# Kernel tuning notes

Hardware: AMD Instinct MI355X
Metric: run time of the kernel (lower is better)

Reference implementation:

```python
import jax, jax.numpy as jnp
import numpy as np
import math

NEG = -1e32
B, S, D, H, DFF, L = 16, 512, 1024, 8, 4096, 3
DK = D // H


def layernorm(x, g, b, eps=1e-5):
    mu = x.mean(-1, keepdims=True)
    var = ((x - mu) ** 2).mean(-1, keepdims=True)
    return (x - mu) / jnp.sqrt(var + eps) * g + b


def gen_dam(alphas, E, bmask):
    # alphas, E: [H, S, 2]; hard gumbel-softmax with straight-through
    Hh, Ss, _ = alphas.shape
    g = -jnp.log(E + 1e-5)
    y_soft = jax.nn.softmax(alphas + g, axis=-1)  # tau = 1
    idx = jnp.argmax(y_soft, axis=-1)
    y_hard = jax.nn.one_hot(idx, 2, dtype=y_soft.dtype)
    m = y_hard - jax.lax.stop_gradient(y_soft) + y_soft
    m = jnp.broadcast_to(m[:, :, 0:1], (Hh, Ss, Ss))
    m = jnp.triu(m)
    m = jnp.rot90(m, 1, axes=(1, 2))
    i = jnp.arange(Ss)[:, None]
    j = jnp.arange(Ss)[None, :]
    src = jnp.clip(j - i, 0, Ss - 1)
    shifted = m[:, jnp.arange(Ss)[:, None], src]  # mask_tri[:, i, j] = m[:, i, j - i]
    mask_tri = jnp.where(j >= i, shifted, 0.0)
    masks = mask_tri + jnp.swapaxes(jnp.triu(mask_tri, 1), 1, 2)
    masks = jnp.triu(masks, bmask)
    return masks


def attention(q, k, v, src_mask, dam, zero_pad, gammas):
    # q,k,v: [B,H,S,dk]; src_mask: [S,S] bool; dam: [H,S,S] bool
    dk = q.shape[-1]
    Ss = q.shape[2]
    scores = jnp.einsum('bhqd,bhkd->bhqk', q, k) / math.sqrt(dk)
    damb = dam[None]          # [1,H,S,S]
    smb = src_mask[None, None]  # [1,1,S,S]
    # NOTE: faithful to the torch code, where the first masked_fill(mask==0)
    # result is overwritten - only dam masks the first softmax.
    sc = jnp.where(damb, scores, NEG)
    sc = jax.nn.softmax(sc, axis=-1)
    sc = sc * smb.astype(sc.dtype) * damb.astype(sc.dtype)
    distcum = jnp.cumsum(sc, axis=-1)
    disttot = jnp.sum(sc, axis=-1, keepdims=True)
    pos = jnp.abs(jnp.arange(Ss)[None, :] - jnp.arange(Ss)[:, None]).astype(scores.dtype)
    dist = jnp.sqrt(jnp.clip((disttot - distcum) * pos[None, None], 0.0, None))
    dist = jax.lax.stop_gradient(dist)
    gamma = -jax.nn.softplus(gammas)[None]  # [1,H,1,1]
    te = jnp.clip(jnp.exp(dist * gamma), 1e-5, 1e5)
    scores = scores * te
    scores = jnp.where(smb, scores, NEG)
    scores = jnp.where(damb, scores, NEG)
    scores = jax.nn.softmax(scores, axis=-1)
    if zero_pad:
        scores = scores.at[:, :, 0, :].set(0.0)
    return jnp.einsum('bhqk,bhkd->bhqd', scores, v)


def transformer_layer(bmask, query, key, values, apply_pos, p):
    Bb, Ss, Dd = query.shape
    Hh = p['gammas'].shape[0]
    dam = gen_dam(p['alphas'], p['E'], bmask) == 0
    src_mask = jnp.triu(jnp.ones((Ss, Ss), jnp.int32), bmask) == 0
    k = (key @ p['kW'].T + p['kb']).reshape(Bb, Ss, Hh, -1).transpose(0, 2, 1, 3)
    q = (query @ p['kW'].T + p['kb']).reshape(Bb, Ss, Hh, -1).transpose(0, 2, 1, 3)  # kq_same
    v = (values @ p['vW'].T + p['vb']).reshape(Bb, Ss, Hh, -1).transpose(0, 2, 1, 3)
    att = attention(q, k, v, src_mask, dam, bmask == 0, p['gammas'])
    concat = att.transpose(0, 2, 1, 3).reshape(Bb, Ss, Dd)
    q2 = concat @ p['oW'].T + p['ob']
    x = layernorm(query + q2, p['ln1_g'], p['ln1_b'])
    if apply_pos:
        ff = jax.nn.relu(x @ p['w1'].T + p['b1']) @ p['w2'].T + p['b2']
        x = layernorm(x + ff, p['ln2_g'], p['ln2_b'])
    return x


def setup_inputs() -> dict:
    key = jax.random.key(0)
    ks = jax.random.split(key, 16)
    sc = 0.02
    return {
        'q_embed_data': jax.random.normal(ks[0], (B, S, D), jnp.float32),
        'qa_embed_data': jax.random.normal(ks[1], (B, S, D), jnp.float32),
        'kW': sc * jax.random.normal(ks[2], (L, D, D), jnp.float32),
        'kb': jnp.zeros((L, D), jnp.float32),
        'vW': sc * jax.random.normal(ks[3], (L, D, D), jnp.float32),
        'vb': jnp.zeros((L, D), jnp.float32),
        'oW': sc * jax.random.normal(ks[4], (L, D, D), jnp.float32),
        'ob': jnp.zeros((L, D), jnp.float32),
        'gammas': 0.5 * jax.random.normal(ks[5], (L, H, 1, 1), jnp.float32),
        'alphas': 0.001 * jax.random.normal(ks[6], (L, H, S, 2), jnp.float32),
        'ln1_g': jnp.ones((L, D), jnp.float32),
        'ln1_b': jnp.zeros((L, D), jnp.float32),
        'w1': sc * jax.random.normal(ks[7], (L, DFF, D), jnp.float32),
        'b1': jnp.zeros((L, DFF), jnp.float32),
        'w2': sc * jax.random.normal(ks[8], (L, D, DFF), jnp.float32),
        'b2': jnp.zeros((L, D), jnp.float32),
        'ln2_g': jnp.ones((L, D), jnp.float32),
        'ln2_b': jnp.zeros((L, D), jnp.float32),
        'gumbel_E': jax.random.exponential(ks[9], (L, H, S, 2), jnp.float32),
    }


def reference(q_embed_data, qa_embed_data, kW, kb, vW, vb, oW, ob, gammas,
              alphas, ln1_g, ln1_b, w1, b1, w2, b2, ln2_g, ln2_b, gumbel_E):
    def P(l):
        return {'kW': kW[l], 'kb': kb[l], 'vW': vW[l], 'vb': vb[l],
                'oW': oW[l], 'ob': ob[l], 'gammas': gammas[l], 'alphas': alphas[l],
                'ln1_g': ln1_g[l], 'ln1_b': ln1_b[l], 'w1': w1[l], 'b1': b1[l],
                'w2': w2[l], 'b2': b2[l], 'ln2_g': ln2_g[l], 'ln2_b': ln2_b[l],
                'E': gumbel_E[l]}
    # blocks_1: self-attention over answer embedding (mask=1)
    y = transformer_layer(1, qa_embed_data, qa_embed_data, qa_embed_data, True, P(0))
    # blocks_2: self-attn on question emb (no FFN), then cross-attn into y
    x = transformer_layer(1, q_embed_data, q_embed_data, q_embed_data, False, P(1))
    x = transformer_layer(0, x, x, y, True, P(2))
    return x
```

## Files before the change

kernel.cpp:

```cpp
#include <hip/hip_runtime.h>
#include <math.h>

#define NEGV -1e32f

typedef __bf16 bf16_t;
typedef _Float16 f16_t;
typedef __bf16 bf16x8 __attribute__((ext_vector_type(8)));
typedef __bf16 bf16x4 __attribute__((ext_vector_type(4)));
typedef _Float16 f16x8 __attribute__((ext_vector_type(8)));
typedef float floatx4 __attribute__((ext_vector_type(4)));

static __device__ __forceinline__ float fexp(float x) { return __expf(x); }
#if __has_builtin(__builtin_amdgcn_sqrtf)
static __device__ __forceinline__ float fsqrt(float x) { return __builtin_amdgcn_sqrtf(x); }
#else
static __device__ __forceinline__ float fsqrt(float x) { return sqrtf(x); }
#endif
#if __has_builtin(__builtin_amdgcn_rcpf)
static __device__ __forceinline__ float frcp(float x) { return __builtin_amdgcn_rcpf(x); }
#else
static __device__ __forceinline__ float frcp(float x) { return 1.0f / x; }
#endif

static __device__ __forceinline__ float wave_sum(float v) {
#pragma unroll
  for (int d = 32; d > 0; d >>= 1) v += __shfl_xor(v, d, 64);
  return v;
}
static __device__ __forceinline__ float wave_max(float v) {
#pragma unroll
  for (int d = 32; d > 0; d >>= 1) v = fmaxf(v, __shfl_xor(v, d, 64));
  return v;
}

static __device__ __forceinline__ void gl2lds16(const bf16_t* g, bf16_t* l) {
  __builtin_amdgcn_global_load_lds((__attribute__((address_space(1))) void*)(void*)g,
                                   (__attribute__((address_space(3))) void*)l, 16, 0, 0);
}

template <int WM, int WN, int FM, int FN, int BIAS_MODE, bool RELU, int OUT_MODE>
__global__ __launch_bounds__(WM * WN * 64) void gemm_db(
    const bf16_t* __restrict__ A, long lda, long a_so, long a_si,
    const bf16_t* __restrict__ B, long ldb, long b_so, long b_si,
    void* __restrict__ Cv, long ldc, long c_so, long c_si,
    const float* __restrict__ bias, int zdiv, int K, float alpha)
{
  constexpr int THREADS = WM * WN * 64;
  constexpr int BM = WM * FM * 16;
  constexpr int BN = WN * FN * 16;
  constexpr int RR = THREADS / 8;
  constexpr int RA = BM / RR;
  constexpr int RB = BN / RR;
  constexpr int NSTG = RA + RB;
  extern __shared__ bf16_t smem[];
  bf16_t* const Asb = smem;
  bf16_t* const Bsb = smem + 2 * (BM * 64);

  const int tid = threadIdx.x;
  const int wave = tid >> 6;
  const int lane = tid & 63;
  const int wm = wave / WN;
  const int wn = wave % WN;
  const int z = blockIdx.z;
  const long zo = z / zdiv;
  const long zi = z % zdiv;
  A += zo * a_so + zi * a_si;
  B += zo * b_so + zi * b_si;
  const long m0 = (long)blockIdx.x * BM;
  const long n0 = (long)blockIdx.y * BN;

  const int srow = tid >> 3;
  const int scol = ((tid & 7) ^ (srow & 7)) * 8;
  const bf16_t* gA = A + (m0 + srow) * lda + scol;
  const bf16_t* gB = B + (n0 + srow) * ldb + scol;
  const int lofs = wave * 512;

  floatx4 acc[FM][FN] = {};
  const int lr = lane & 15;
  const int kg = lane >> 4;
  const int NT = K >> 6;

  {
    bf16_t* lA = Asb + lofs;
    bf16_t* lB = Bsb + lofs;
#pragma unroll
    for (int r = 0; r < RA; ++r) gl2lds16(gA + (long)(r * RR) * lda, lA + r * RR * 64);
#pragma unroll
    for (int r = 0; r < RB; ++r) gl2lds16(gB + (long)(r * RR) * ldb, lB + r * RR * 64);
  }

  for (int t = 0; t < NT; ++t) {
    const int buf = t & 1;
    if (t + 1 < NT) {
      const long ko = (long)(t + 1) * 64;
      bf16_t* lA = Asb + (buf ^ 1) * (BM * 64) + lofs;
      bf16_t* lB = Bsb + (buf ^ 1) * (BN * 64) + lofs;
#pragma unroll
      for (int r = 0; r < RA; ++r) gl2lds16(gA + (long)(r * RR) * lda + ko, lA + r * RR * 64);
#pragma unroll
      for (int r = 0; r < RB; ++r) gl2lds16(gB + (long)(r * RR) * ldb + ko, lB + r * RR * 64);
      asm volatile("s_waitcnt vmcnt(%0)" :: "n"(NSTG) : "memory");
    } else {
      asm volatile("s_waitcnt vmcnt(0)" ::: "memory");
    }
    __builtin_amdgcn_s_barrier();
    __builtin_amdgcn_sched_barrier(0);
    const bf16_t* __restrict__ Ab = Asb + buf * (BM * 64);
    const bf16_t* __restrict__ Bb = Bsb + buf * (BN * 64);
#pragma unroll
    for (int h = 0; h < 2; ++h) {
      const int slot = ((h * 4 + kg) ^ (lr & 7)) * 8;
      bf16x8 af[FM], bfr[FN];
#pragma unroll
      for (int m = 0; m < FM; ++m)
        af[m] = *(const bf16x8*)(Ab + (wm * (FM * 16) + m * 16 + lr) * 64 + slot);
#pragma unroll
      for (int n = 0; n < FN; ++n)
        bfr[n] = *(const bf16x8*)(Bb + (wn * (FN * 16) + n * 16 + lr) * 64 + slot);
#pragma unroll
      for (int m = 0; m < FM; ++m)
#pragma unroll
        for (int n = 0; n < FN; ++n)
          acc[m][n] = __builtin_amdgcn_mfma_f32_16x16x32_bf16(af[m], bfr[n], acc[m][n], 0, 0, 0);
    }
    __builtin_amdgcn_sched_barrier(0);
    __builtin_amdgcn_s_barrier();
  }

  const long coff = zo * c_so + zi * c_si;
  const int q4 = (lane >> 4) * 4;
#pragma unroll
  for (int m = 0; m < FM; ++m) {
#pragma unroll
    for (int n = 0; n < FN; ++n) {
#pragma unroll
      for (int r = 0; r < 4; ++r) {
        const long row = m0 + wm * (FM * 16) + m * 16 + q4 + r;
        const long col = n0 + wn * (FN * 16) + n * 16 + lr;
        float v = acc[m][n][r] * alpha;
        if (BIAS_MODE == 1) v += bias[col];
        if (BIAS_MODE == 2) v += bias[row];
        if (RELU) v = fmaxf(v, 0.0f);
        const long idx = coff + row * ldc + col;
        if (OUT_MODE == 1)      ((bf16_t*)Cv)[idx] = (bf16_t)v;
        else if (OUT_MODE == 2) ((f16_t*)Cv)[idx]  = (f16_t)v;
        else                    ((float*)Cv)[idx]  = v;
      }
    }
  }
}

template <int BIAS_MODE, bool RELU, int OUT_MODE>
__global__ __launch_bounds__(256) void gemm_bt(
    const bf16_t* __restrict__ A, long lda, long a_so, long a_si,
    const bf16_t* __restrict__ B, long ldb, long b_so, long b_si,
    void* __restrict__ Cv, long ldc, long c_so, long c_si,
    const float* __restrict__ bias, int zdiv, int K, float alpha)
{
  __shared__ bf16_t As[8192];
  __shared__ bf16_t Bs[8192];
  const int tid = threadIdx.x;
  const int wave = tid >> 6;
  const int lane = tid & 63;
  const int wr = wave >> 1;
  const int wc = wave & 1;
  const int z = blockIdx.z;
  const long zo = z / zdiv;
  const long zi = z % zdiv;
  A += zo * a_so + zi * a_si;
  B += zo * b_so + zi * b_si;
  const long m0 = (long)blockIdx.x * 128;
  const long n0 = (long)blockIdx.y * 128;

  const int srow = tid >> 3;
  const int scol = ((tid & 7) ^ (srow & 7)) * 8;
  const bf16_t* gA = A + (m0 + srow) * lda + scol;
  const bf16_t* gB = B + (n0 + srow) * ldb + scol;
  bf16_t* lA = As + wave * 512;
  bf16_t* lB = Bs + wave * 512;

  floatx4 acc[4][4] = {};
  const int lr = lane & 15;
  const int kg = lane >> 4;

  for (int k0 = 0; k0 < K; k0 += 64) {
#pragma unroll
    for (int r = 0; r < 4; ++r) {
      gl2lds16(gA + (long)r * 32 * lda + k0, lA + r * 2048);
      gl2lds16(gB + (long)r * 32 * ldb + k0, lB + r * 2048);
    }
    __syncthreads();
#pragma unroll
    for (int h = 0; h < 2; ++h) {
      const int slot = ((h * 4 + kg) ^ (lr & 7)) * 8;
      bf16x8 af[4], bfr[4];
#pragma unroll
      for (int t = 0; t < 4; ++t) {
        af[t]  = *(const bf16x8*)(As + (wr * 64 + t * 16 + lr) * 64 + slot);
        bfr[t] = *(const bf16x8*)(Bs + (wc * 64 + t * 16 + lr) * 64 + slot);
      }
#pragma unroll
      for (int tm = 0; tm < 4; ++tm)
#pragma unroll
        for (int tn = 0; tn < 4; ++tn)
          acc[tm][tn] = __builtin_amdgcn_mfma_f32_16x16x32_bf16(af[tm], bfr[tn], acc[tm][tn], 0, 0, 0);
    }
    __syncthreads();
  }

  const long coff = zo * c_so + zi * c_si;
  const int q4 = (lane >> 4) * 4;
#pragma unroll
  for (int tm = 0; tm < 4; ++tm) {
#pragma unroll
    for (int tn = 0; tn < 4; ++tn) {
#pragma unroll
      for (int r = 0; r < 4; ++r) {
        const long row = m0 + wr * 64 + tm * 16 + q4 + r;
        const long col = n0 + wc * 64 + tn * 16 + lr;
        float v = acc[tm][tn][r] * alpha;
        if (BIAS_MODE == 1) v += bias[col];
        if (BIAS_MODE == 2) v += bias[row];
        if (RELU) v = fmaxf(v, 0.0f);
        const long idx = coff + row * ldc + col;
        if (OUT_MODE == 1)      ((bf16_t*)Cv)[idx] = (bf16_t)v;
        else if (OUT_MODE == 2) ((f16_t*)Cv)[idx]  = (f16_t)v;
        else                    ((float*)Cv)[idx]  = v;
      }
    }
  }
}

__global__ __launch_bounds__(256) void cast_kernel(const float* __restrict__ in,
                                                   bf16_t* __restrict__ out, long n)
{
  const long i = ((long)blockIdx.x * 256 + threadIdx.x) * 4;
  if (i >= n) return;
  const float4 v = *(const float4*)(in + i);
  bf16x4 o;
  o[0] = (bf16_t)v.x; o[1] = (bf16_t)v.y; o[2] = (bf16_t)v.z; o[3] = (bf16_t)v.w;
  *(bf16x4*)(out + i) = o;
}

__global__ void bbit_kernel(const float* __restrict__ alphas, const float* __restrict__ E,
                            int* __restrict__ bbit, int n)
{
  const int i = blockIdx.x * 256 + threadIdx.x;
  if (i >= n) return;
  const float l0 = alphas[2 * i]     - logf(E[2 * i]     + 1e-5f);
  const float l1 = alphas[2 * i + 1] - logf(E[2 * i + 1] + 1e-5f);
  bbit[i] = (l0 >= l1) ? 1 : 0;
}

template <bool XBF>
__global__ __launch_bounds__(256) void ln_kernel(
    const void* __restrict__ Xv, const float* __restrict__ R,
    const float* __restrict__ g, const float* __restrict__ b,
    float* __restrict__ out32, bf16_t* __restrict__ out16)
{
  const long row = blockIdx.x;
  const int t = threadIdx.x;
  float x0, x1, x2, x3;
  if (XBF) {
    const bf16x4 xv = *(const bf16x4*)((const bf16_t*)Xv + row * 1024 + t * 4);
    x0 = (float)xv[0]; x1 = (float)xv[1]; x2 = (float)xv[2]; x3 = (float)xv[3];
  } else {
    const float4 xv = *(const float4*)((const float*)Xv + row * 1024 + t * 4);
    x0 = xv.x; x1 = xv.y; x2 = xv.z; x3 = xv.w;
  }
  const float4 rv = *(const float4*)(R + row * 1024 + t * 4);
  const float v0 = x0 + rv.x, v1 = x1 + rv.y, v2 = x2 + rv.z, v3 = x3 + rv.w;
  float s  = v0 + v1 + v2 + v3;
  float s2 = v0 * v0 + v1 * v1 + v2 * v2 + v3 * v3;
  s = wave_sum(s); s2 = wave_sum(s2);
  __shared__ float red[8];
  const int wv = t >> 6, lane = t & 63;
  if (lane == 0) { red[wv] = s; red[4 + wv] = s2; }
  __syncthreads();
  s  = red[0] + red[1] + red[2] + red[3];
  s2 = red[4] + red[5] + red[6] + red[7];
  const float mu = s * (1.0f / 1024.0f);
  const float var = s2 * (1.0f / 1024.0f) - mu * mu;
  const float rstd = rsqrtf(var + 1e-5f);
  const float4 gv = *(const float4*)(g + t * 4);
  const float4 bv = *(const float4*)(b + t * 4);
  float4 ov;
  ov.x = (v0 - mu) * rstd * gv.x + bv.x;
  ov.y = (v1 - mu) * rstd * gv.y + bv.y;
  ov.z = (v2 - mu) * rstd * gv.z + bv.z;
  ov.w = (v3 - mu) * rstd * gv.w + bv.w;
  if (out32) *(float4*)(out32 + row * 1024 + t * 4) = ov;
  if (out16) {
    bf16x4 oh;
    oh[0] = (bf16_t)ov.x; oh[1] = (bf16_t)ov.y; oh[2] = (bf16_t)ov.z; oh[3] = (bf16_t)ov.w;
    *(bf16x4*)(out16 + row * 1024 + t * 4) = oh;
  }
}

__global__ __launch_bounds__(256) void attn_mid(
    const f16_t* __restrict__ S, bf16_t* __restrict__ P,
    const int* __restrict__ bbit, const float* __restrict__ gam,
    const int bmask, const int zero_pad)
{
  const int wid = threadIdx.x >> 6;
  const int lane = threadIdx.x & 63;
  const long rowid = (long)blockIdx.x * 4 + wid;
  const int i = (int)(rowid & 511);
  const int h = (int)(rowid >> 9) & 7;
  const f16_t* s = S + rowid * 512;
  const int jb = lane * 8;

  const float gv = gam[h];
  const float gamma = -log1pf(fexp(gv));

  float sv[8];
  {
    const f16x8 a = *(const f16x8*)(s + jb);
#pragma unroll
    for (int u = 0; u < 8; ++u) sv[u] = (float)a[u];
  }
  const int* bb = bbit + h * 512;
  float z[8];
  bool band[8];
  float m1 = NEGV;
#pragma unroll
  for (int u = 0; u < 8; ++u) {
    const int j = jb + u;
    const bool bd = j < i + bmask;
    band[u] = bd;
    int d = j - i; d = d < 0 ? 0 : d;
    const bool allowed = bd || (bb[d] == 0);
    z[u] = allowed ? sv[u] : NEGV;
    m1 = fmaxf(m1, z[u]);
  }
  m1 = wave_max(m1);
  float e[8], es = 0.f;
#pragma unroll
  for (int u = 0; u < 8; ++u) { e[u] = fexp(z[u] - m1); es += e[u]; }
  es = wave_sum(es);
  const float inv1 = frcp(es);

  float c[8];
  float run = 0.f;
#pragma unroll
  for (int u = 0; u < 8; ++u) {
    const float p = band[u] ? e[u] * inv1 : 0.f;
    run += p;
    c[u] = run;
  }
  float x = run;
#pragma unroll
  for (int d = 1; d < 64; d <<= 1) {
    const float y = __shfl_up(x, (unsigned)d, 64);
    if (lane >= d) x += y;
  }
  const float tot = __shfl(x, 63, 64);
  const float ex = x - run;

  float z2[8];
  float m2 = NEGV;
#pragma unroll
  for (int u = 0; u < 8; ++u) {
    const int j = jb + u;
    const float cc = c[u] + ex;
    const float pos = fabsf((float)(i - j));
    const float dist = fsqrt(fmaxf((tot - cc) * pos, 0.f));
    float te = fexp(dist * gamma);
    te = fminf(fmaxf(te, 1e-5f), 1e5f);
    z2[u] = band[u] ? sv[u] * te : NEGV;
    m2 = fmaxf(m2, z2[u]);
  }
  m2 = wave_max(m2);
  float f[8], es2 = 0.f;
#pragma unroll
  for (int u = 0; u < 8; ++u) { f[u] = fexp(z2[u] - m2); es2 += f[u]; }
  es2 = wave_sum(es2);
  const float inv2 = (zero_pad && i == 0) ? 0.f : frcp(es2);
  bf16x8 o;
#pragma unroll
  for (int u = 0; u < 8; ++u) o[u] = (bf16_t)(f[u] * inv2);
  *(bf16x8*)(P + rowid * 512 + jb) = o;
}

extern "C" void kernel_launch(void* const* d_in, const int* in_sizes, int n_in,
                              void* d_out, int out_size, void* d_ws, size_t ws_size,
                              hipStream_t stream)
{
  (void)in_sizes; (void)n_in; (void)out_size; (void)ws_size;
  const float* q_emb  = (const float*)d_in[0];
  const float* qa_emb = (const float*)d_in[1];
  const float* kW = (const float*)d_in[2];
  const float* kb = (const float*)d_in[3];
  const float* vW = (const float*)d_in[4];
  const float* vb = (const float*)d_in[5];
  const float* oW = (const float*)d_in[6];
  const float* ob = (const float*)d_in[7];
  const float* gammas = (const float*)d_in[8];
  const float* alphas = (const float*)d_in[9];
  const float* ln1_g = (const float*)d_in[10];
  const float* ln1_b = (const float*)d_in[11];
  const float* w1 = (const float*)d_in[12];
  const float* b1 = (const float*)d_in[13];
  const float* w2 = (const float*)d_in[14];
  const float* b2 = (const float*)d_in[15];
  const float* ln2_g = (const float*)d_in[16];
  const float* ln2_b = (const float*)d_in[17];
  const float* gumE = (const float*)d_in[18];
  float* outp = (float*)d_out;

  static bool attr_done = false;
  if (!attr_done) {
    attr_done = true;
    (void)hipFuncSetAttribute(reinterpret_cast<const void*>(&gemm_db<2,2,4,4,1,false,1>),
                              hipFuncAttributeMaxDynamicSharedMemorySize, 65536);
    (void)hipFuncSetAttribute(reinterpret_cast<const void*>(&gemm_db<2,2,4,4,2,false,1>),
                              hipFuncAttributeMaxDynamicSharedMemorySize, 65536);
    (void)hipFuncSetAttribute(reinterpret_cast<const void*>(&gemm_db<2,2,4,4,0,false,1>),
                              hipFuncAttributeMaxDynamicSharedMemorySize, 65536);
    (void)hipFuncSetAttribute(reinterpret_cast<const void*>(&gemm_db<2,2,4,4,1,false,0>),
                              hipFuncAttributeMaxDynamicSharedMemorySize, 65536);
    (void)hipFuncSetAttribute(reinterpret_cast<const void*>(&gemm_db<2,4,8,4,1,true,1>),
                              hipFuncAttributeMaxDynamicSharedMemorySize, 131072);
  }

  const size_t MBc = 1ull << 20;
  char* W = (char*)d_ws;
  int*    bbit = (int*)W;
  bf16_t* VB   = (bf16_t*)(W + 1 * MBc);
  bf16_t* XB   = (bf16_t*)(W + 17 * MBc);
  bf16_t* kWb  = (bf16_t*)(W + 33 * MBc);
  bf16_t* vWb  = (bf16_t*)(W + 39 * MBc);
  bf16_t* oWb  = (bf16_t*)(W + 45 * MBc);
  bf16_t* w1b  = (bf16_t*)(W + 51 * MBc);
  bf16_t* w2b  = (bf16_t*)(W + 59 * MBc);
  bf16_t* KQB  = (bf16_t*)(W + 67 * MBc);
  bf16_t* VT   = (bf16_t*)(W + 83 * MBc);
  f16_t*  SSPP = (f16_t*)(W + 99 * MBc);
  bf16_t* PPb  = (bf16_t*)(W + 99 * MBc);
  bf16_t* ATT  = (bf16_t*)(W + 163 * MBc);
  float*  O32  = (float*)(W + 67 * MBc);
  bf16_t* X1B  = (bf16_t*)(W + 99 * MBc);
  bf16_t* H1B  = (bf16_t*)(W + 115 * MBc);

  const long ND = 8388608;

  auto run_layer = [&](int l, const void* Qin, bool qin_bf16, const bf16_t* XBp,
                       const bf16_t* VBp, bool apply_pos, int bmask,
                       float* o32, bf16_t* o16) {
    const bf16_t* kWl = kWb + (long)l * 1048576;
    const bf16_t* vWl = vWb + (long)l * 1048576;
    const bf16_t* oWl = oWb + (long)l * 1048576;
    gemm_db<2,2,4,4,1,false,1><<<dim3(64, 8, 1), dim3(256), 65536, stream>>>(
        XBp, 1024, 0, 0, kWl, 1024, 0, 0, (void*)KQB, 1024, 0, 0,
        kb + l * 1024, 1, 1024, 1.0f);
    gemm_db<2,2,4,4,2,false,1><<<dim3(8, 4, 16), dim3(256), 65536, stream>>>(
        vWl, 1024, 0, 0, VBp, 1024, 524288, 0, (void*)VT, 512, 524288, 0,
        vb + l * 1024, 1, 1024, 1.0f);
    const int zp = (bmask == 0) ? 1 : 0;
    gemm_bt<0, false, 2><<<dim3(4, 4, 128), dim3(256), 0, stream>>>(
        KQB, 1024, 524288, 128, KQB, 1024, 524288, 128,
        (void*)SSPP, 512, 2097152, 262144, nullptr, 8, 128, 0.08838834764831845f);
    attn_mid<<<dim3(16384), dim3(256), 0, stream>>>(
        SSPP, PPb, bbit + l * 4096, gammas + l * 8, bmask, zp);
    gemm_db<2,2,4,4,0,false,1><<<dim3(4, 1, 128), dim3(256), 65536, stream>>>(
        PPb, 512, 2097152, 262144, VT, 512, 524288, 65536,
        (void*)ATT, 1024, 524288, 128, nullptr, 8, 512, 1.0f);
    gemm_db<2,2,4,4,1,false,0><<<dim3(64, 8, 1), dim3(256), 65536, stream>>>(
        ATT, 1024, 0, 0, oWl, 1024, 0, 0, (void*)O32, 1024, 0, 0,
        ob + l * 1024, 1, 1024, 1.0f);
    if (!apply_pos) {
      if (qin_bf16)
        ln_kernel<true><<<dim3(8192), dim3(256), 0, stream>>>(
            Qin, O32, ln1_g + l * 1024, ln1_b + l * 1024, o32, o16);
      else
        ln_kernel<false><<<dim3(8192), dim3(256), 0, stream>>>(
            Qin, O32, ln1_g + l * 1024, ln1_b + l * 1024, o32, o16);
    } else {
      cast_kernel<<<dim3(4096), dim3(256), 0, stream>>>(w1 + (long)l * 4194304, w1b, 4194304);
      cast_kernel<<<dim3(4096), dim3(256), 0, stream>>>(w2 + (long)l * 4194304, w2b, 4194304);
      if (qin_bf16)
        ln_kernel<true><<<dim3(8192), dim3(256), 0, stream>>>(
            Qin, O32, ln1_g + l * 1024, ln1_b + l * 1024, nullptr, X1B);
      else
        ln_kernel<false><<<dim3(8192), dim3(256), 0, stream>>>(
            Qin, O32, ln1_g + l * 1024, ln1_b + l * 1024, nullptr, X1B);
      gemm_db<2,4,8,4,1,true,1><<<dim3(32, 16, 1), dim3(512), 131072, stream>>>(
          X1B, 1024, 0, 0, w1b, 1024, 0, 0, (void*)H1B, 4096, 0, 0,
          b1 + l * 4096, 1, 1024, 1.0f);
      gemm_db<2,2,4,4,1,false,0><<<dim3(64, 8, 1), dim3(256), 65536, stream>>>(
          H1B, 4096, 0, 0, w2b, 4096, 0, 0, (void*)O32, 1024, 0, 0,
          b2 + l * 1024, 1, 4096, 1.0f);
      ln_kernel<true><<<dim3(8192), dim3(256), 0, stream>>>(
          X1B, O32, ln2_g + l * 1024, ln2_b + l * 1024, o32, o16);
    }
  };

  bbit_kernel<<<dim3(48), dim3(256), 0, stream>>>(alphas, gumE, bbit, 12288);
  cast_kernel<<<dim3(3072), dim3(256), 0, stream>>>(kW, kWb, 3145728);
  cast_kernel<<<dim3(3072), dim3(256), 0, stream>>>(vW, vWb, 3145728);
  cast_kernel<<<dim3(3072), dim3(256), 0, stream>>>(oW, oWb, 3145728);

  cast_kernel<<<dim3(8192), dim3(256), 0, stream>>>(qa_emb, XB, ND);
  run_layer(0, qa_emb, false, XB, XB, true, 1, nullptr, VB);
  cast_kernel<<<dim3(8192), dim3(256), 0, stream>>>(q_emb, XB, ND);
  run_layer(1, q_emb, false, XB, XB, false, 1, nullptr, XB);
  run_layer(2, XB, true, XB, VB, true, 0, outp, nullptr);
}
```

Measured before the change: 1.109 ms.

## Interleave global-to-LDS prefetch rounds with MFMA phases in GEMM main loop

```diff
diff --git a/kernel.cpp b/kernel.cpp
--- a/kernel.cpp
+++ b/kernel.cpp
@@ -52,6 +52,9 @@
   constexpr int RA = BM / RR;
   constexpr int RB = BN / RR;
   constexpr int NSTG = RA + RB;
+  constexpr int MG = (FM >= 8) ? 2 : 1;
+  constexpr int MSUB = FM / MG;
+  constexpr int PH = 2 * MG;
   extern __shared__ bf16_t smem[];
   bf16_t* const Asb = smem;
   bf16_t* const Bsb = smem + 2 * (BM * 64);
@@ -80,26 +83,26 @@
   const int kg = lane >> 4;
   const int NT = K >> 6;
 
-  {
-    bf16_t* lA = Asb + lofs;
-    bf16_t* lB = Bsb + lofs;
-#pragma unroll
-    for (int r = 0; r < RA; ++r) gl2lds16(gA + (long)(r * RR) * lda, lA + r * RR * 64);
-#pragma unroll
-    for (int r = 0; r < RB; ++r) gl2lds16(gB + (long)(r * RR) * ldb, lB + r * RR * 64);
-  }
+  auto stage_round = [&](int q, long ko, int dstbuf) {
+    if (q < RA)
+      gl2lds16(gA + (long)(q * RR) * lda + ko,
+               Asb + dstbuf * (BM * 64) + lofs + q * RR * 64);
+    else
+      gl2lds16(gB + (long)((q - RA) * RR) * ldb + ko,
+               Bsb + dstbuf * (BN * 64) + lofs + (q - RA) * RR * 64);
+  };
+
+#pragma unroll
+  for (int q = 0; q < NSTG; ++q) stage_round(q, 0, 0);
 
   for (int t = 0; t < NT; ++t) {
     const int buf = t & 1;
-    if (t + 1 < NT) {
-      const long ko = (long)(t + 1) * 64;
-      bf16_t* lA = Asb + (buf ^ 1) * (BM * 64) + lofs;
-      bf16_t* lB = Bsb + (buf ^ 1) * (BN * 64) + lofs;
-#pragma unroll
-      for (int r = 0; r < RA; ++r) gl2lds16(gA + (long)(r * RR) * lda + ko, lA + r * RR * 64);
-#pragma unroll
-      for (int r = 0; r < RB; ++r) gl2lds16(gB + (long)(r * RR) * ldb + ko, lB + r * RR * 64);
-      asm volatile("s_waitcnt vmcnt(%0)" :: "n"(NSTG) : "memory");
+    const bool pf = (t + 1 < NT);
+    const long ko = (long)(t + 1) * 64;
+    if (pf) {
+#pragma unroll
+      for (int q = 0; q < 2; ++q) stage_round(q, ko, buf ^ 1);
+      asm volatile("s_waitcnt vmcnt(2)" ::: "memory");
     } else {
       asm volatile("s_waitcnt vmcnt(0)" ::: "memory");
     }
@@ -110,21 +113,39 @@
 #pragma unroll
     for (int h = 0; h < 2; ++h) {
       const int slot = ((h * 4 + kg) ^ (lr & 7)) * 8;
-      bf16x8 af[FM], bfr[FN];
-#pragma unroll
-      for (int m = 0; m < FM; ++m)
-        af[m] = *(const bf16x8*)(Ab + (wm * (FM * 16) + m * 16 + lr) * 64 + slot);
-#pragma unroll
-      for (int n = 0; n < FN; ++n)
-        bfr[n] = *(const bf16x8*)(Bb + (wn * (FN * 16) + n * 16 + lr) * 64 + slot);
-#pragma unroll
-      for (int m = 0; m < FM; ++m)
-#pragma unroll
-        for (int n = 0; n < FN; ++n)
-          acc[m][n] = __builtin_amdgcn_mfma_f32_16x16x32_bf16(af[m], bfr[n], acc[m][n], 0, 0, 0);
-    }
-    __builtin_amdgcn_sched_barrier(0);
-    __builtin_amdgcn_s_barrier();
+      bf16x8 bfr[FN];
+#pragma unroll
+      for (int g = 0; g < MG; ++g) {
+        const int pi = h * MG + g;
+        bf16x8 af[MSUB];
+#pragma unroll
+        for (int m = 0; m < MSUB; ++m)
+          af[m] = *(const bf16x8*)(Ab + (wm * (FM * 16) + (g * MSUB + m) * 16 + lr) * 64 + slot);
+        if (g == 0) {
+#pragma unroll
+          for (int n = 0; n < FN; ++n)
+            bfr[n] = *(const bf16x8*)(Bb + (wn * (FN * 16) + n * 16 + lr) * 64 + slot);
+        }
+        if (pf) {
+          const int q0 = 2 + pi * 6 / PH;
+          const int q1 = 2 + (pi + 1) * 6 / PH;
+#pragma unroll
+          for (int q = q0; q < q1; ++q) stage_round(q, ko, buf ^ 1);
+        }
+        asm volatile("s_waitcnt lgkmcnt(0)" ::: "memory");
+        __builtin_amdgcn_sched_barrier(0);
+        __builtin_amdgcn_s_setprio(1);
+#pragma unroll
+        for (int m = 0; m < MSUB; ++m)
+#pragma unroll
+          for (int n = 0; n < FN; ++n)
+            acc[g * MSUB + m][n] =
+                __builtin_amdgcn_mfma_f32_16x16x32_bf16(af[m], bfr[n], acc[g * MSUB + m][n], 0, 0, 0);
+        __builtin_amdgcn_s_setprio(0);
+        __builtin_amdgcn_sched_barrier(0);
+        __builtin_amdgcn_s_barrier();
+      }
+    }
   }
 
   const long coff = zo * c_so + zi * c_si;
```

Result: no change. 1.099 ms, median of 2 (-0.9%).
